# Kernel optimization log

Hardware: AMD Instinct MI355X
Metric: run time of the kernel (lower is better)

Reference implementation:

```python
import jax, jax.numpy as jnp
import numpy as np

T, N, H, W = 1, 2048, 512, 512
CHUNK = 128  # gaussians per scan step; intermediate alpha is (CHUNK,H,W) ~ 128MB fp32


def setup_inputs() -> dict:
    key = jax.random.key(0)
    k1, k2, k3, k4 = jax.random.split(key, 4)
    # matches torch init: atanh(2*(rand-0.5)) so tanh(xyz) is uniform in (-1,1)
    u = jax.random.uniform(k1, (T, N, 2), dtype=jnp.float32, minval=1e-4, maxval=1.0 - 1e-4)
    xyz = jnp.arctanh(2.0 * (u - 0.5))
    # cholesky params near identity: [1,0,1] + 0.01*randn
    cholesky = jnp.array([1.0, 0.0, 1.0], jnp.float32).reshape(1, 1, 3) \
        + 0.01 * jax.random.normal(k2, (T, N, 3), dtype=jnp.float32)
    opacity = jnp.ones((N, 1), jnp.float32)
    features_dc = jax.random.normal(k4, (N, 3), dtype=jnp.float32)
    return {"xyz": xyz, "cholesky": cholesky, "opacity": opacity,
            "features_dc": features_dc, "frame_index": 0}


def _render_frame(means, chol, colors, opac):
    """Accumulated-summation 2D Gaussian splat (GaussianImage rasterize_gaussians_sum).

    means: (N,2) in (-1,1); chol: (N,3) Cholesky elems (l11,l21,l22);
    colors: (N,3) in (0,1); opac: (N,) in (0,1). Returns (3,H,W).
    """
    l1, l2, l3 = chol[:, 0], chol[:, 1], chol[:, 2]
    # Sigma = L L^T with L = [[l1,0],[l2,l3]]
    s11 = l1 * l1
    s12 = l1 * l2
    s22 = l2 * l2 + l3 * l3
    det = s11 * s22 - s12 * s12
    conic = jnp.stack([s22 / det, -s12 / det, s11 / det], axis=-1)  # (N,3) inverse cov
    # project to pixel coords
    xys = 0.5 * (means + 1.0) * jnp.array([W, H], means.dtype)  # (N,2)

    px = jnp.arange(W, dtype=means.dtype) + 0.5  # pixel centers
    py = jnp.arange(H, dtype=means.dtype) + 0.5

    steps = N // CHUNK
    xs = (xys.reshape(steps, CHUNK, 2), conic.reshape(steps, CHUNK, 3),
          colors.reshape(steps, CHUNK, 3), opac.reshape(steps, CHUNK))

    def body(img, args):
        xy, cc, col, op = args
        dx = xy[:, 0, None] - px[None, :]          # (C,W)
        dy = xy[:, 1, None] - py[None, :]          # (C,H)
        sigma = (0.5 * cc[:, 0, None, None] * (dx[:, None, :] ** 2)
                 + 0.5 * cc[:, 2, None, None] * (dy[:, :, None] ** 2)
                 + cc[:, 1, None, None] * dy[:, :, None] * dx[:, None, :])  # (C,H,W)
        alpha = op[:, None, None] * jnp.exp(-sigma)
        alpha = jnp.where(sigma < 0.0, 0.0, jnp.minimum(alpha, 0.999))
        alpha = jnp.where(alpha < 1.0 / 255.0, 0.0, alpha)  # kernel skip threshold
        img = img + jnp.einsum('chw,ck->khw', alpha, col)
        return img, None

    img0 = jnp.zeros((3, H, W), means.dtype)
    img, _ = jax.lax.scan(body, img0, xs)
    return img


def reference(xyz, cholesky, opacity, features_dc, frame_index):
    cholesky_bound = jnp.array([0.5, 0.0, 0.5], xyz.dtype)
    means_t = jnp.tanh(xyz[frame_index])                       # (N,2)
    chol_t = cholesky[frame_index] + cholesky_bound            # (N,3)
    colors = jax.nn.sigmoid(features_dc)                       # (N,3)
    opac = jax.nn.sigmoid(opacity[:, 0])                       # (N,)
    img = _render_frame(means_t, chol_t, colors, opac)
    img = jnp.clip(img, 0.0, 1.0)
    return img[None]  # (1,3,H,W)
```

## Files before the change

kernel.cpp:

```cpp
#include <hip/hip_runtime.h>
#include <math.h>

#define N_GAUSS 2048
#define IMG_H 512
#define IMG_W 512
#define TILE_W 64
#define TILE_H 4
#define TILES_X (IMG_W / TILE_W)
#define TILES_Y (IMG_H / TILE_H)
#define N_TILES (TILES_X * TILES_Y)
#define PCACHE 512

__global__ __launch_bounds__(256) void splat_tiled(
    const float* __restrict__ xyz,
    const float* __restrict__ chol,
    const float* __restrict__ opacity,
    const float* __restrict__ fdc,
    float* __restrict__ out)
{
    __shared__ int   s_count;
    __shared__ int   s_idx[N_GAUSS];
    __shared__ float s_par[PCACHE][9];

    const int tile = blockIdx.x;
    const int tx = tile % TILES_X;
    const int ty = tile / TILES_X;
    const int t  = threadIdx.x;

    const float x0 = (float)(tx * TILE_W) + 0.5f;
    const float x1 = (float)(tx * TILE_W + TILE_W - 1) + 0.5f;
    const float y0 = (float)(ty * TILE_H) + 0.5f;
    const float y1 = (float)(ty * TILE_H + TILE_H - 1) + 0.5f;

    if (t == 0) s_count = 0;
    __syncthreads();

    for (int g = t; g < N_GAUSS; g += 256) {
        float mx = tanhf(xyz[2 * g]);
        float my = tanhf(xyz[2 * g + 1]);
        float cx = 0.5f * (mx + 1.0f) * (float)IMG_W;
        float cy = 0.5f * (my + 1.0f) * (float)IMG_H;

        float l1 = chol[3 * g]     + 0.5f;
        float l2 = chol[3 * g + 1];
        float l3 = chol[3 * g + 2] + 0.5f;
        float s11 = l1 * l1;
        float s22 = l2 * l2 + l3 * l3;

        float op = 1.0f / (1.0f + __expf(-opacity[g]));
        float smax = __logf(255.0f * op);
        if (smax <= 0.0f) continue;

        float rx = sqrtf(2.0f * smax * s11) + 1.0f;
        float ry = sqrtf(2.0f * smax * s22) + 1.0f;

        if (cx + rx < x0 || cx - rx > x1 || cy + ry < y0 || cy - ry > y1)
            continue;

        int pos = atomicAdd(&s_count, 1);
        s_idx[pos] = g;
        if (pos < PCACHE) {
            float s12 = l1 * l2;
            float det = s11 * s22 - s12 * s12;
            float inv = 1.0f / det;
            s_par[pos][0] = cx;
            s_par[pos][1] = cy;
            s_par[pos][2] =  s22 * inv;
            s_par[pos][3] = -s12 * inv;
            s_par[pos][4] =  s11 * inv;
            s_par[pos][5] = 1.0f / (1.0f + expf(-opacity[g]));
            s_par[pos][6] = 1.0f / (1.0f + expf(-fdc[3 * g]));
            s_par[pos][7] = 1.0f / (1.0f + expf(-fdc[3 * g + 1]));
            s_par[pos][8] = 1.0f / (1.0f + expf(-fdc[3 * g + 2]));
        }
    }
    __syncthreads();

    const int w = tx * TILE_W + (t & (TILE_W - 1));
    const int h = ty * TILE_H + (t >> 6);
    const float px = (float)w + 0.5f;
    const float py = (float)h + 0.5f;

    float R = 0.0f, G = 0.0f, B = 0.0f;
    const int cnt = s_count;
    for (int i = 0; i < cnt; i++) {
        float cx, cy, c0, c1, c2, op, cr, cg, cb;
        if (i < PCACHE) {
            cx = s_par[i][0]; cy = s_par[i][1];
            c0 = s_par[i][2]; c1 = s_par[i][3]; c2 = s_par[i][4];
            op = s_par[i][5];
            cr = s_par[i][6]; cg = s_par[i][7]; cb = s_par[i][8];
        } else {
            int g = s_idx[i];
            float mx = tanhf(xyz[2 * g]);
            float my = tanhf(xyz[2 * g + 1]);
            cx = 0.5f * (mx + 1.0f) * (float)IMG_W;
            cy = 0.5f * (my + 1.0f) * (float)IMG_H;
            float l1 = chol[3 * g]     + 0.5f;
            float l2 = chol[3 * g + 1];
            float l3 = chol[3 * g + 2] + 0.5f;
            float s11 = l1 * l1;
            float s12 = l1 * l2;
            float s22 = l2 * l2 + l3 * l3;
            float det = s11 * s22 - s12 * s12;
            float inv = 1.0f / det;
            c0 =  s22 * inv; c1 = -s12 * inv; c2 = s11 * inv;
            op = 1.0f / (1.0f + expf(-opacity[g]));
            cr = 1.0f / (1.0f + expf(-fdc[3 * g]));
            cg = 1.0f / (1.0f + expf(-fdc[3 * g + 1]));
            cb = 1.0f / (1.0f + expf(-fdc[3 * g + 2]));
        }
        float dx = cx - px;
        float dy = cy - py;
        float sigma = 0.5f * c0 * dx * dx + 0.5f * c2 * dy * dy + c1 * dy * dx;
        if (sigma < 0.0f) continue;
        float alpha = fminf(op * expf(-sigma), 0.999f);
        if (alpha < (1.0f / 255.0f)) continue;
        R += alpha * cr;
        G += alpha * cg;
        B += alpha * cb;
    }

    const int p = h * IMG_W + w;
    out[p]                     = fminf(fmaxf(R, 0.0f), 1.0f);
    out[IMG_H * IMG_W + p]     = fminf(fmaxf(G, 0.0f), 1.0f);
    out[2 * IMG_H * IMG_W + p] = fminf(fmaxf(B, 0.0f), 1.0f);
}

extern "C" void kernel_launch(void* const* d_in, const int* in_sizes, int n_in,
                              void* d_out, int out_size, void* d_ws, size_t ws_size,
                              hipStream_t stream) {
    const float* xyz     = (const float*)d_in[0];
    const float* chol    = (const float*)d_in[1];
    const float* opacity = (const float*)d_in[2];
    const float* fdc     = (const float*)d_in[3];

    float* out = (float*)d_out;

    splat_tiled<<<N_TILES, 256, 0, stream>>>(xyz, chol, opacity, fdc, out);
}
```

Baseline: 79.64 us.

## Precompute gaussian params and bounding boxes in a separate prep kernel

Adds a prep kernel that computes each gaussian's centre, conic, opacity, colour and screen bounding box once and writes them to workspace as float4 records. The tile kernel then only tests the precomputed bounding boxes for culling and reads parameters from global memory (L2-cached) per gaussian, instead of recomputing tanh/exp per tile and caching them in shared memory. This removes redundant transcendental work across 1024 tiles but adds a second launch and replaces LDS reads in the inner loop with global float4 loads indexed indirectly.

After: 75.29 us. 1.06x faster.

```diff
diff --git a/kernel.cpp b/kernel.cpp
--- a/kernel.cpp
+++ b/kernel.cpp
@@ -9,18 +9,63 @@
 #define TILES_X (IMG_W / TILE_W)
 #define TILES_Y (IMG_H / TILE_H)
 #define N_TILES (TILES_X * TILES_Y)
-#define PCACHE 512
 
-__global__ __launch_bounds__(256) void splat_tiled(
+
+__global__ __launch_bounds__(256) void prep_kernel(
     const float* __restrict__ xyz,
     const float* __restrict__ chol,
     const float* __restrict__ opacity,
     const float* __restrict__ fdc,
+    float4* __restrict__ ws)
+{
+    int g = blockIdx.x * 256 + threadIdx.x;
+    if (g >= N_GAUSS) return;
+
+    float mx = tanhf(xyz[2 * g]);
+    float my = tanhf(xyz[2 * g + 1]);
+    float cx = 0.5f * (mx + 1.0f) * (float)IMG_W;
+    float cy = 0.5f * (my + 1.0f) * (float)IMG_H;
+
+    float l1 = chol[3 * g]     + 0.5f;
+    float l2 = chol[3 * g + 1];
+    float l3 = chol[3 * g + 2] + 0.5f;
+    float s11 = l1 * l1;
+    float s12 = l1 * l2;
+    float s22 = l2 * l2 + l3 * l3;
+    float det = s11 * s22 - s12 * s12;
+    float inv = 1.0f / det;
+    float c0 =  s22 * inv;
+    float c1 = -s12 * inv;
+    float c2 =  s11 * inv;
+
+    float op = 1.0f / (1.0f + expf(-opacity[g]));
+    float cr = 1.0f / (1.0f + expf(-fdc[3 * g]));
+    float cg = 1.0f / (1.0f + expf(-fdc[3 * g + 1]));
+    float cb = 1.0f / (1.0f + expf(-fdc[3 * g + 2]));
+
+    float smax = logf(255.0f * op);
+    float bx0, bx1, by0, by1;
+    if (smax <= 0.0f) {
+        bx0 = 1.0f; bx1 = 0.0f; by0 = 1.0f; by1 = 0.0f;
+    } else {
+        float rx = sqrtf(2.0f * smax * s11) + 1.0f;
+        float ry = sqrtf(2.0f * smax * s22) + 1.0f;
+        bx0 = cx - rx; bx1 = cx + rx;
+        by0 = cy - ry; by1 = cy + ry;
+    }
+
+    ws[g * 4 + 0] = make_float4(cx, cy, c0, c1);
+    ws[g * 4 + 1] = make_float4(c2, op, cr, cg);
+    ws[g * 4 + 2] = make_float4(cb, 0.0f, 0.0f, 0.0f);
+    ws[g * 4 + 3] = make_float4(bx0, bx1, by0, by1);
+}
+
+__global__ __launch_bounds__(256) void splat_tiled(
+    const float4* __restrict__ ws,
     float* __restrict__ out)
 {
-    __shared__ int   s_count;
-    __shared__ int   s_idx[N_GAUSS];
-    __shared__ float s_par[PCACHE][9];
+    __shared__ int s_count;
+    __shared__ int s_idx[N_GAUSS];
 
     const int tile = blockIdx.x;
     const int tx = tile % TILES_X;
@@ -35,43 +80,13 @@
     if (t == 0) s_count = 0;
     __syncthreads();
 
-    for (int g = t; g < N_GAUSS; g += 256) {
-        float mx = tanhf(xyz[2 * g]);
-        float my = tanhf(xyz[2 * g + 1]);
-        float cx = 0.5f * (mx + 1.0f) * (float)IMG_W;
-        float cy = 0.5f * (my + 1.0f) * (float)IMG_H;
-
-        float l1 = chol[3 * g]     + 0.5f;
-        float l2 = chol[3 * g + 1];
-        float l3 = chol[3 * g + 2] + 0.5f;
-        float s11 = l1 * l1;
-        float s22 = l2 * l2 + l3 * l3;
-
-        float op = 1.0f / (1.0f + __expf(-opacity[g]));
-        float smax = __logf(255.0f * op);
-        if (smax <= 0.0f) continue;
-
-        float rx = sqrtf(2.0f * smax * s11) + 1.0f;
-        float ry = sqrtf(2.0f * smax * s22) + 1.0f;
-
-        if (cx + rx < x0 || cx - rx > x1 || cy + ry < y0 || cy - ry > y1)
-            continue;
-
-        int pos = atomicAdd(&s_count, 1);
-        s_idx[pos] = g;
-        if (pos < PCACHE) {
-            float s12 = l1 * l2;
-            float det = s11 * s22 - s12 * s12;
-            float inv = 1.0f / det;
-            s_par[pos][0] = cx;
-            s_par[pos][1] = cy;
-            s_par[pos][2] =  s22 * inv;
-            s_par[pos][3] = -s12 * inv;
-            s_par[pos][4] =  s11 * inv;
-            s_par[pos][5] = 1.0f / (1.0f + expf(-opacity[g]));
-            s_par[pos][6] = 1.0f / (1.0f + expf(-fdc[3 * g]));
-            s_par[pos][7] = 1.0f / (1.0f + expf(-fdc[3 * g + 1]));
-            s_par[pos][8] = 1.0f / (1.0f + expf(-fdc[3 * g + 2]));
+    #pragma unroll
+    for (int k = 0; k < N_GAUSS / 256; k++) {
+        int g = k * 256 + t;
+        float4 bb = ws[g * 4 + 3];
+        if (bb.x <= x1 && bb.y >= x0 && bb.z <= y1 && bb.w >= y0) {
+            int pos = atomicAdd(&s_count, 1);
+            s_idx[pos] = g;
         }
     }
     __syncthreads();
@@ -84,41 +99,19 @@
     float R = 0.0f, G = 0.0f, B = 0.0f;
     const int cnt = s_count;
     for (int i = 0; i < cnt; i++) {
-        float cx, cy, c0, c1, c2, op, cr, cg, cb;
-        if (i < PCACHE) {
-            cx = s_par[i][0]; cy = s_par[i][1];
-            c0 = s_par[i][2]; c1 = s_par[i][3]; c2 = s_par[i][4];
-            op = s_par[i][5];
-            cr = s_par[i][6]; cg = s_par[i][7]; cb = s_par[i][8];
-        } else {
-            int g = s_idx[i];
-            float mx = tanhf(xyz[2 * g]);
-            float my = tanhf(xyz[2 * g + 1]);
-            cx = 0.5f * (mx + 1.0f) * (float)IMG_W;
-            cy = 0.5f * (my + 1.0f) * (float)IMG_H;
-            float l1 = chol[3 * g]     + 0.5f;
-            float l2 = chol[3 * g + 1];
-            float l3 = chol[3 * g + 2] + 0.5f;
-            float s11 = l1 * l1;
-            float s12 = l1 * l2;
-            float s22 = l2 * l2 + l3 * l3;
-            float det = s11 * s22 - s12 * s12;
-            float inv = 1.0f / det;
-            c0 =  s22 * inv; c1 = -s12 * inv; c2 = s11 * inv;
-            op = 1.0f / (1.0f + expf(-opacity[g]));
-            cr = 1.0f / (1.0f + expf(-fdc[3 * g]));
-            cg = 1.0f / (1.0f + expf(-fdc[3 * g + 1]));
-            cb = 1.0f / (1.0f + expf(-fdc[3 * g + 2]));
-        }
-        float dx = cx - px;
-        float dy = cy - py;
-        float sigma = 0.5f * c0 * dx * dx + 0.5f * c2 * dy * dy + c1 * dy * dx;
+        int g = s_idx[i];
+        float4 q0 = ws[g * 4 + 0];
+        float4 q1 = ws[g * 4 + 1];
+        float4 q2 = ws[g * 4 + 2];
+        float dx = q0.x - px;
+        float dy = q0.y - py;
+        float sigma = 0.5f * q0.z * dx * dx + 0.5f * q1.x * dy * dy + q0.w * dy * dx;
         if (sigma < 0.0f) continue;
-        float alpha = fminf(op * expf(-sigma), 0.999f);
+        float alpha = fminf(q1.y * expf(-sigma), 0.999f);
         if (alpha < (1.0f / 255.0f)) continue;
-        R += alpha * cr;
-        G += alpha * cg;
-        B += alpha * cb;
+        R += alpha * q1.z;
+        G += alpha * q1.w;
+        B += alpha * q2.x;
     }
 
     const int p = h * IMG_W + w;
@@ -135,7 +128,9 @@
     const float* opacity = (const float*)d_in[2];
     const float* fdc     = (const float*)d_in[3];
 
-    float* out = (float*)d_out;
+    float4* wsp = (float4*)d_ws;
+    float* out  = (float*)d_out;
 
-    splat_tiled<<<N_TILES, 256, 0, stream>>>(xyz, chol, opacity, fdc, out);
+    prep_kernel<<<N_GAUSS / 256, 256, 0, stream>>>(xyz, chol, opacity, fdc, wsp);
+    splat_tiled<<<N_TILES, 256, 0, stream>>>(wsp, out);
 }
```
